# Kernel optimization log

Measured on AMD Instinct MI355X. Metric: run time of the kernel, lower is better.

The kernel has to match this reference:

```python
import jax, jax.numpy as jnp
import numpy as np

B, N, D, H = 8, 1024, 1024, 16
HD = D // H  # head_size = 64


def setup_inputs() -> dict:
    key = jax.random.key(0)
    k0, k1, k2, k3, k4 = jax.random.split(key, 5)
    scale = 1.0 / np.sqrt(D)
    return {
        "x": jax.random.normal(k0, (B, N, D), dtype=jnp.float32),
        "Wqkv": jax.random.normal(k1, (D, 3 * D), dtype=jnp.float32) * scale,
        "bqkv": jnp.zeros((3 * D,), dtype=jnp.float32),
        "Wo": jax.random.normal(k2, (D, D), dtype=jnp.float32) * scale,
        "bo": jnp.zeros((D,), dtype=jnp.float32),
    }


def reference(x, Wqkv, bqkv, Wo, bo):
    # Fused QKV projection: [B, N, 3D]
    qkv = jnp.einsum("bnd,de->bne", x, Wqkv) + bqkv
    q, k, v = jnp.split(qkv, 3, axis=-1)

    def split_heads(t):  # [B, N, D] -> [B, H, N, HD]
        return t.reshape(B, N, H, HD).transpose(0, 2, 1, 3)

    q, k, v = split_heads(q), split_heads(k), split_heads(v)

    # Scaled dot-product attention (no mask, dropout=0)
    scores = jnp.einsum("bhqd,bhkd->bhqk", q, k) / jnp.sqrt(jnp.float32(HD))
    alpha = jax.nn.softmax(scores, axis=-1)
    ctx = jnp.einsum("bhqk,bhkd->bhqd", alpha, v)  # [B, H, N, HD]

    ctx = ctx.transpose(0, 2, 1, 3).reshape(B, N, D)
    out = jnp.einsum("bnd,de->bne", ctx, Wo) + bo
    return out
```

## Files before the change

kernel.cpp:

```cpp
#include <hip/hip_runtime.h>
#include <cstdint>
#include <cstddef>

typedef _Float16 half_t;
typedef __attribute__((ext_vector_type(4))) _Float16 half4v;
typedef __attribute__((ext_vector_type(8))) _Float16 half8v;
typedef __attribute__((ext_vector_type(4))) float float4v;
typedef __attribute__((ext_vector_type(16))) float float16v;
typedef __attribute__((ext_vector_type(4))) unsigned uint4v;
typedef __attribute__((ext_vector_type(2))) int int2v;

typedef __attribute__((address_space(1))) const void gv_t;
typedef __attribute__((address_space(3))) void lv_t;

__device__ __forceinline__ void lds_cp16(const void* g, void* l) {
  __builtin_amdgcn_global_load_lds((gv_t*)g, (lv_t*)l, 16, 0, 0);
}

__device__ __forceinline__ unsigned pkh(float a, float b) {
  return __builtin_bit_cast(unsigned, __builtin_amdgcn_cvt_pkrtz(a, b));
}

__global__ __launch_bounds__(256) void k_cvt(const float* __restrict__ in,
                                             half_t* __restrict__ out) {
  int i = blockIdx.x * 256 + threadIdx.x;
  float4 v = ((const float4*)in)[i];
  half4v h = {(half_t)v.x, (half_t)v.y, (half_t)v.z, (half_t)v.w};
  ((half4v*)out)[i] = h;
}

__global__ __launch_bounds__(256) void k_tcvt(const float* __restrict__ in,
                                              half_t* __restrict__ out, int R, int C) {
  __shared__ float t[32][33];
  int c0 = blockIdx.x * 32, r0 = blockIdx.y * 32;
  int tc = threadIdx.x & 31, tr = threadIdx.x >> 5;
#pragma unroll
  for (int i = 0; i < 4; i++)
    t[tr + i * 8][tc] = in[(size_t)(r0 + tr + i * 8) * C + c0 + tc];
  __syncthreads();
#pragma unroll
  for (int i = 0; i < 4; i++)
    out[(size_t)(c0 + tr + i * 8) * R + r0 + tc] = (half_t)t[tc][tr + i * 8];
}

__global__ __launch_bounds__(256, 3) void k_qkv(
    const half_t* __restrict__ A, const half_t* __restrict__ Bt,
    const float* __restrict__ bias,
    half_t* __restrict__ Qo, half_t* __restrict__ Ko, half_t* __restrict__ Vo) {
  __shared__ half_t Bs[2][128 * 64];
  const int tid = threadIdx.x;
  const int lane = tid & 63;
  const int w = tid >> 6;
  const int xcd = blockIdx.x & 7;
  const int l = blockIdx.x >> 3;
  const int nc = l >> 6, r = l & 63;
  const int m0 = (xcd * 8 + (r >> 3)) * 128;
  const int n0 = (nc * 8 + (r & 7)) * 128;
  const int wr = w >> 1, wc = w & 1;
  const int fr = lane & 15, fg = lane >> 4;

  int sr[4], sg[4];
#pragma unroll
  for (int j = 0; j < 4; ++j) {
    const int G = j * 256 + tid;
    sr[j] = G >> 3;
    sg[j] = (G & 7) ^ (sr[j] & 7);
  }

  const half_t* Ap = A + (size_t)(m0 + wr * 64 + fr) * 1024 + fg * 8;

  float4v acc[4][4] = {};
  const int so0 = fg ^ (fr & 7);
  const int so1 = (4 | fg) ^ (fr & 7);
  const int brow = wc * 64 + fr;

  half8v a0[8], a1[8];
#pragma unroll
  for (int j = 0; j < 4; ++j)
    lds_cp16(Bt + (size_t)(n0 + sr[j]) * 1024 + sg[j] * 8, &Bs[0][(j * 256 + tid) * 8]);
#pragma unroll
  for (int m = 0; m < 4; ++m)
#pragma unroll
    for (int kk = 0; kk < 2; ++kk)
      a0[m * 2 + kk] = *(const half8v*)(Ap + m * 16384 + kk * 32);
  asm volatile("s_waitcnt vmcnt(0)" ::: "memory");
  __builtin_amdgcn_s_barrier();

#define QKV_ITER(t, cb, ac, an)                                                  \
  do {                                                                           \
    if ((t) + 1 < 16) {                                                          \
      const int kn = ((t) + 1) * 64;                                             \
      _Pragma("unroll") for (int j = 0; j < 4; ++j)                              \
          lds_cp16(Bt + (size_t)(n0 + sr[j]) * 1024 + kn + sg[j] * 8,            \
                   &Bs[(cb) ^ 1][(j * 256 + tid) * 8]);                          \
      _Pragma("unroll") for (int m = 0; m < 4; ++m)                              \
          _Pragma("unroll") for (int kk = 0; kk < 2; ++kk)                       \
              an[m * 2 + kk] = *(const half8v*)(Ap + m * 16384 + kn + kk * 32);  \
    }                                                                            \
    _Pragma("unroll") for (int kk = 0; kk < 2; ++kk) {                           \
      half8v b[4];                                                               \
      _Pragma("unroll") for (int n = 0; n < 4; ++n) {                            \
        const int row = (brow + n * 16) * 64;                                    \
        b[n] = *(const half8v*)(&Bs[cb][row + (kk ? so1 : so0) * 8]);            \
      }                                                                          \
      _Pragma("unroll") for (int m = 0; m < 4; ++m)                              \
          _Pragma("unroll") for (int n = 0; n < 4; ++n)                          \
              acc[m][n] = __builtin_amdgcn_mfma_f32_16x16x32_f16(                \
                  ac[m * 2 + kk], b[n], acc[m][n], 0, 0, 0);                     \
    }                                                                            \
    asm volatile("s_waitcnt vmcnt(0)" ::: "memory");                             \
    __builtin_amdgcn_s_barrier();                                                \
  } while (0)

  for (int tp = 0; tp < 8; ++tp) {
    QKV_ITER(2 * tp, 0, a0, a1);
    QKV_ITER(2 * tp + 1, 1, a1, a0);
  }
#undef QKV_ITER

  const int rq = (lane >> 4) * 4;
  const int cc = lane & 15;
#pragma unroll
  for (int n = 0; n < 4; n++) {
    const int e = n0 + wc * 64 + n * 16 + cc;
    const float bv = bias[e];
    const int which = e >> 10, h = (e >> 6) & 15, hd = e & 63;
#pragma unroll
    for (int m = 0; m < 4; m++) {
      const int rowb = m0 + wr * 64 + m * 16 + rq;
#pragma unroll
      for (int r2 = 0; r2 < 4; r2++) {
        const int row = rowb + r2;
        const int b_ = row >> 10, tok = row & 1023;
        const half_t hv = (half_t)(acc[m][n][r2] + bv);
        const size_t bh = (size_t)(b_ * 16 + h);
        if (which == 0)
          Qo[(bh * 1024 + tok) * 64 + hd] = hv;
        else if (which == 1)
          Ko[(bh * 1024 + tok) * 64 + hd] = hv;
        else
          Vo[(bh * 64 + hd) * 1024 + tok] = hv;
      }
    }
  }
}

__global__ __launch_bounds__(256, 2) void k_gemm_o(
    const half_t* __restrict__ A, const half_t* __restrict__ Bt,
    const float* __restrict__ bias, float* __restrict__ Cout, int N, int K) {
  __shared__ half_t As[2][128 * 64];
  __shared__ half_t Bs[2][128 * 64];
  const int tid = threadIdx.x;
  const int lane = tid & 63;
  const int w = tid >> 6;
  const int xcd = blockIdx.x & 7;
  const int l = blockIdx.x >> 3;
  const int nc = l >> 6, r = l & 63;
  const int m0 = (xcd * 8 + (r >> 3)) * 128;
  const int n0 = (nc * 8 + (r & 7)) * 128;
  const int wr = w >> 1, wc = w & 1;

  int sr[4], sg[4];
#pragma unroll
  for (int j = 0; j < 4; ++j) {
    const int G = j * 256 + tid;
    sr[j] = G >> 3;
    sg[j] = (G & 7) ^ (sr[j] & 7);
  }

  float4v acc[4][4] = {};
  const int fr = lane & 15;
  const int fg = lane >> 4;
  const int so0 = fg ^ (fr & 7);
  const int so1 = (4 | fg) ^ (fr & 7);
  const int arow = wr * 64 + fr;
  const int brow = wc * 64 + fr;

  const int NT = K >> 6;
#pragma unroll
  for (int j = 0; j < 4; ++j) {
    lds_cp16(A + (size_t)(m0 + sr[j]) * K + sg[j] * 8, &As[0][(j * 256 + tid) * 8]);
    lds_cp16(Bt + (size_t)(n0 + sr[j]) * K + sg[j] * 8, &Bs[0][(j * 256 + tid) * 8]);
  }

  for (int t = 0; t < NT; t++) {
    asm volatile("s_waitcnt vmcnt(0)" ::: "memory");
    __builtin_amdgcn_s_barrier();
    __builtin_amdgcn_sched_barrier(0);
    const int cb = t & 1;
    if (t + 1 < NT) {
      const int kn = (t + 1) * 64;
#pragma unroll
      for (int j = 0; j < 4; ++j) {
        lds_cp16(A + (size_t)(m0 + sr[j]) * K + kn + sg[j] * 8,
                 &As[cb ^ 1][(j * 256 + tid) * 8]);
        lds_cp16(Bt + (size_t)(n0 + sr[j]) * K + kn + sg[j] * 8,
                 &Bs[cb ^ 1][(j * 256 + tid) * 8]);
      }
    }
    half8v a[4][2], b[4][2];
#pragma unroll
    for (int m = 0; m < 4; m++) {
      const int row = (arow + m * 16) * 64;
      a[m][0] = *(const half8v*)(&As[cb][row + so0 * 8]);
      a[m][1] = *(const half8v*)(&As[cb][row + so1 * 8]);
    }
#pragma unroll
    for (int n = 0; n < 4; n++) {
      const int row = (brow + n * 16) * 64;
      b[n][0] = *(const half8v*)(&Bs[cb][row + so0 * 8]);
      b[n][1] = *(const half8v*)(&Bs[cb][row + so1 * 8]);
    }
#pragma unroll
    for (int kk = 0; kk < 2; kk++)
#pragma unroll
      for (int m = 0; m < 4; m++)
#pragma unroll
        for (int n = 0; n < 4; n++)
          acc[m][n] = __builtin_amdgcn_mfma_f32_16x16x32_f16(a[m][kk], b[n][kk],
                                                             acc[m][n], 0, 0, 0);
  }

  const int rq = (lane >> 4) * 4;
  const int cc = lane & 15;
#pragma unroll
  for (int n = 0; n < 4; n++) {
    int e = n0 + wc * 64 + n * 16 + cc;
    float bv = bias[e];
#pragma unroll
    for (int m = 0; m < 4; m++) {
      int rowb = m0 + wr * 64 + m * 16 + rq;
#pragma unroll
      for (int r2 = 0; r2 < 4; r2++)
        Cout[(size_t)(rowb + r2) * N + e] = acc[m][n][r2] + bv;
    }
  }
}

__global__ __launch_bounds__(512, 4) void k_attn(const half_t* __restrict__ Qh,
                                                 const half_t* __restrict__ Kh,
                                                 const half_t* __restrict__ Vt,
                                                 half_t* __restrict__ ctx) {
  __shared__ alignas(16) half_t Ks[2][64 * 64];
  __shared__ alignas(16) half_t Vs[2][64 * 64];
  const int lane = threadIdx.x & 63;
  const int w = threadIdx.x >> 6;
  const int ql = lane & 31, hi = lane >> 5;
  const int xcd = blockIdx.x & 7, loc = blockIdx.x >> 3;
  const int bh = xcd * 16 + (loc >> 2), qb = loc & 3;
  const int b_ = bh >> 4, h = bh & 15;
  const int q0 = qb * 256 + w * 32;

  const half_t* Qp = Qh + (size_t)bh * (1024 * 64);
  const half_t* Kp = Kh + (size_t)bh * (1024 * 64);
  const half_t* Vp = Vt + (size_t)bh * (64 * 1024);

  half8v qf[4];
#pragma unroll
  for (int c = 0; c < 4; c++) {
    half8v tq = *(const half8v*)(Qp + (size_t)(q0 + ql) * 64 + c * 16 + hi * 8);
    qf[c] = tq * (_Float16)0.125f;
  }

  const int G = w * 64 + lane;
  const int rS = G >> 3;
  const int gS = (G & 7) ^ (rS & 7);

  float16v co[2] = {};
  float mr = -1e30f, ssum = 0.f;

  lds_cp16(Kp + (size_t)rS * 64 + gS * 8, &Ks[0][w * 512]);
  lds_cp16(Vp + (size_t)rS * 1024 + 0 + gS * 8, &Vs[0][w * 512]);
  __syncthreads();

  int cur = 0;
  for (int t = 0; t < 16; t++) {
    if (t < 15) {
      const int kn = (t + 1) * 64;
      lds_cp16(Kp + (size_t)(kn + rS) * 64 + gS * 8, &Ks[cur ^ 1][w * 512]);
      lds_cp16(Vp + (size_t)rS * 1024 + kn + gS * 8, &Vs[cur ^ 1][w * 512]);
    }

    float16v sacc[2] = {};
    __builtin_amdgcn_s_setprio(1);
#pragma unroll
    for (int c = 0; c < 4; c++)
#pragma unroll
      for (int s = 0; s < 2; s++) {
        int row = s * 32 + ql;
        half8v kf = *(const half8v*)(&Ks[cur][row * 64 + (((2 * c + hi) ^ (row & 7)) * 8)]);
        sacc[s] = __builtin_amdgcn_mfma_f32_32x32x16_f16(kf, qf[c], sacc[s], 0, 0, 0);
      }
    __builtin_amdgcn_s_setprio(0);

    float mx = -1e30f;
#pragma unroll
    for (int s = 0; s < 2; s++)
#pragma unroll
      for (int i = 0; i < 16; i++) mx = fmaxf(mx, sacc[s][i]);
    mx = fmaxf(mx, __shfl_xor(mx, 32, 64));
    if (mx > mr + 8.f) {
      float fac = __expf(mr - mx);
      mr = mx;
      ssum *= fac;
#pragma unroll
      for (int dd = 0; dd < 2; dd++)
#pragma unroll
        for (int i = 0; i < 16; i++) co[dd][i] *= fac;
    }
    float rsum = 0.f;
#pragma unroll
    for (int s = 0; s < 2; s++)
#pragma unroll
      for (int i = 0; i < 16; i++) {
        float e = __expf(sacc[s][i] - mr);
        sacc[s][i] = e;
        rsum += e;
      }
    rsum += __shfl_xor(rsum, 32, 64);
    ssum += rsum;

#pragma unroll
    for (int kc = 0; kc < 4; kc++) {
      const int s = kc >> 1, o = (kc & 1) * 8;
      unsigned dA0 = pkh(sacc[s][o + 0], sacc[s][o + 1]);
      unsigned dA1 = pkh(sacc[s][o + 2], sacc[s][o + 3]);
      unsigned dB0 = pkh(sacc[s][o + 4], sacc[s][o + 5]);
      unsigned dB1 = pkh(sacc[s][o + 6], sacc[s][o + 7]);
      int2v r0 = __builtin_amdgcn_permlane32_swap((int)dA0, (int)dB0, false, false);
      int2v r1 = __builtin_amdgcn_permlane32_swap((int)dA1, (int)dB1, false, false);
      uint4v pw = {(unsigned)r0.x, (unsigned)r1.x, (unsigned)r0.y, (unsigned)r1.y};
      half8v pf = __builtin_bit_cast(half8v, pw);
      __builtin_amdgcn_s_setprio(1);
#pragma unroll
      for (int dd = 0; dd < 2; dd++) {
        int row = dd * 32 + ql;
        half8v vf = *(const half8v*)(&Vs[cur][row * 64 + (((2 * kc + hi) ^ (row & 7)) * 8)]);
        co[dd] = __builtin_amdgcn_mfma_f32_32x32x16_f16(vf, pf, co[dd], 0, 0, 0);
      }
      __builtin_amdgcn_s_setprio(0);
    }
    __syncthreads();
    cur ^= 1;
  }

  float rinv = 1.0f / ssum;
  half_t* outp = ctx + ((size_t)(b_ * 1024 + q0 + ql) * 1024 + h * 64);
#pragma unroll
  for (int dd = 0; dd < 2; dd++)
#pragma unroll
    for (int g = 0; g < 4; g++) {
      int d0 = dd * 32 + g * 8 + hi * 4;
      unsigned p0 = pkh(co[dd][g * 4 + 0] * rinv, co[dd][g * 4 + 1] * rinv);
      unsigned p1 = pkh(co[dd][g * 4 + 2] * rinv, co[dd][g * 4 + 3] * rinv);
      *(unsigned*)(outp + d0) = p0;
      *(unsigned*)(outp + d0 + 2) = p1;
    }
}

extern "C" void kernel_launch(void* const* d_in, const int* in_sizes, int n_in,
                              void* d_out, int out_size, void* d_ws, size_t ws_size,
                              hipStream_t stream) {
  const float* x = (const float*)d_in[0];
  const float* Wqkv = (const float*)d_in[1];
  const float* bqkv = (const float*)d_in[2];
  const float* Wo = (const float*)d_in[3];
  const float* bo = (const float*)d_in[4];
  float* out = (float*)d_out;
  char* ws = (char*)d_ws;

  const size_t NEED = 75497472;
  if (ws_size < NEED) return;
  half_t* xh = (half_t*)(ws);
  half_t* wqkvT = (half_t*)(ws + 16777216);
  half_t* woT = (half_t*)(ws + 23068672);
  half_t* Qh = (half_t*)(ws + 25165824);
  half_t* Kh = (half_t*)(ws + 41943040);
  half_t* Vt = (half_t*)(ws + 58720256);
  half_t* ctxh = xh;

  k_cvt<<<8192, 256, 0, stream>>>(x, xh);
  k_tcvt<<<dim3(96, 32), 256, 0, stream>>>(Wqkv, wqkvT, 1024, 3072);
  k_tcvt<<<dim3(32, 32), 256, 0, stream>>>(Wo, woT, 1024, 1024);
  k_qkv<<<1536, 256, 0, stream>>>(xh, wqkvT, bqkv, Qh, Kh, Vt);
  k_attn<<<512, 512, 0, stream>>>(Qh, Kh, Vt, ctxh);
  k_gemm_o<<<512, 256, 0, stream>>>(ctxh, woT, bo, out, 1024, 1024);
}
```

Baseline: 211.9 us.

## Make QKV GEMM persistent over three N tiles with LDS-staged A

The QKV projection kernel now launches 512 blocks instead of 1536, and each block loops over three 128-wide output column tiles for the same 128-row A tile. A is staged through double-buffered LDS with global_load_lds instead of going straight to registers, and results are written out after every 16 K-steps. MFMA sections in both GEMMs are wrapped with s_setprio to favour the compute phase. The aim is better L2 reuse of A and fewer waves in flight, at the cost of lower occupancy (launch bounds drop to 2 blocks per CU) and a longer serial loop per block.

After: 172.0 us. 1.23x faster.

```diff
diff --git a/kernel.cpp b/kernel.cpp
--- a/kernel.cpp
+++ b/kernel.cpp
@@ -43,19 +43,19 @@
     out[(size_t)(c0 + tr + i * 8) * R + r0 + tc] = (half_t)t[tc][tr + i * 8];
 }
 
-__global__ __launch_bounds__(256, 3) void k_qkv(
+__global__ __launch_bounds__(256, 2) void k_qkv(
     const half_t* __restrict__ A, const half_t* __restrict__ Bt,
     const float* __restrict__ bias,
     half_t* __restrict__ Qo, half_t* __restrict__ Ko, half_t* __restrict__ Vo) {
+  __shared__ half_t As[2][128 * 64];
   __shared__ half_t Bs[2][128 * 64];
   const int tid = threadIdx.x;
   const int lane = tid & 63;
   const int w = tid >> 6;
   const int xcd = blockIdx.x & 7;
-  const int l = blockIdx.x >> 3;
-  const int nc = l >> 6, r = l & 63;
-  const int m0 = (xcd * 8 + (r >> 3)) * 128;
-  const int n0 = (nc * 8 + (r & 7)) * 128;
+  const int loc = blockIdx.x >> 3;
+  const int m0 = (xcd * 8 + (loc & 7)) * 128;
+  const int nbase = loc >> 3;
   const int wr = w >> 1, wc = w & 1;
   const int fr = lane & 15, fg = lane >> 4;
 
@@ -67,80 +67,92 @@
     sg[j] = (G & 7) ^ (sr[j] & 7);
   }
 
-  const half_t* Ap = A + (size_t)(m0 + wr * 64 + fr) * 1024 + fg * 8;
-
   float4v acc[4][4] = {};
+
   const int so0 = fg ^ (fr & 7);
   const int so1 = (4 | fg) ^ (fr & 7);
+  const int arow = wr * 64 + fr;
   const int brow = wc * 64 + fr;
-
-  half8v a0[8], a1[8];
-#pragma unroll
-  for (int j = 0; j < 4; ++j)
-    lds_cp16(Bt + (size_t)(n0 + sr[j]) * 1024 + sg[j] * 8, &Bs[0][(j * 256 + tid) * 8]);
-#pragma unroll
-  for (int m = 0; m < 4; ++m)
-#pragma unroll
-    for (int kk = 0; kk < 2; ++kk)
-      a0[m * 2 + kk] = *(const half8v*)(Ap + m * 16384 + kk * 32);
-  asm volatile("s_waitcnt vmcnt(0)" ::: "memory");
-  __builtin_amdgcn_s_barrier();
-
-#define QKV_ITER(t, cb, ac, an)                                                  \
-  do {                                                                           \
-    if ((t) + 1 < 16) {                                                          \
-      const int kn = ((t) + 1) * 64;                                             \
-      _Pragma("unroll") for (int j = 0; j < 4; ++j)                              \
-          lds_cp16(Bt + (size_t)(n0 + sr[j]) * 1024 + kn + sg[j] * 8,            \
-                   &Bs[(cb) ^ 1][(j * 256 + tid) * 8]);                          \
-      _Pragma("unroll") for (int m = 0; m < 4; ++m)                              \
-          _Pragma("unroll") for (int kk = 0; kk < 2; ++kk)                       \
-              an[m * 2 + kk] = *(const half8v*)(Ap + m * 16384 + kn + kk * 32);  \
-    }                                                                            \
-    _Pragma("unroll") for (int kk = 0; kk < 2; ++kk) {                           \
-      half8v b[4];                                                               \
-      _Pragma("unroll") for (int n = 0; n < 4; ++n) {                            \
-        const int row = (brow + n * 16) * 64;                                    \
-        b[n] = *(const half8v*)(&Bs[cb][row + (kk ? so1 : so0) * 8]);            \
-      }                                                                          \
-      _Pragma("unroll") for (int m = 0; m < 4; ++m)                              \
-          _Pragma("unroll") for (int n = 0; n < 4; ++n)                          \
-              acc[m][n] = __builtin_amdgcn_mfma_f32_16x16x32_f16(                \
-                  ac[m * 2 + kk], b[n], acc[m][n], 0, 0, 0);                     \
-    }                                                                            \
-    asm volatile("s_waitcnt vmcnt(0)" ::: "memory");                             \
-    __builtin_amdgcn_s_barrier();                                                \
-  } while (0)
-
-  for (int tp = 0; tp < 8; ++tp) {
-    QKV_ITER(2 * tp, 0, a0, a1);
-    QKV_ITER(2 * tp + 1, 1, a1, a0);
-  }
-#undef QKV_ITER
-
   const int rq = (lane >> 4) * 4;
   const int cc = lane & 15;
-#pragma unroll
-  for (int n = 0; n < 4; n++) {
-    const int e = n0 + wc * 64 + n * 16 + cc;
-    const float bv = bias[e];
-    const int which = e >> 10, h = (e >> 6) & 15, hd = e & 63;
+
+#pragma unroll
+  for (int j = 0; j < 4; ++j) {
+    lds_cp16(A + (size_t)(m0 + sr[j]) * 1024 + sg[j] * 8, &As[0][(j * 256 + tid) * 8]);
+    lds_cp16(Bt + (size_t)(nbase * 128 + sr[j]) * 1024 + sg[j] * 8,
+             &Bs[0][(j * 256 + tid) * 8]);
+  }
+
+  for (int T = 0; T < 48; ++T) {
+    asm volatile("s_waitcnt vmcnt(0)" ::: "memory");
+    __builtin_amdgcn_s_barrier();
+    __builtin_amdgcn_sched_barrier(0);
+    const int cb = T & 1;
+    if (T + 1 < 48) {
+      const int Tn = T + 1;
+      const int kn = (Tn & 15) * 64;
+      const int n0n = (nbase + (Tn >> 4) * 8) * 128;
+#pragma unroll
+      for (int j = 0; j < 4; ++j) {
+        lds_cp16(A + (size_t)(m0 + sr[j]) * 1024 + kn + sg[j] * 8,
+                 &As[cb ^ 1][(j * 256 + tid) * 8]);
+        lds_cp16(Bt + (size_t)(n0n + sr[j]) * 1024 + kn + sg[j] * 8,
+                 &Bs[cb ^ 1][(j * 256 + tid) * 8]);
+      }
+    }
+    half8v a[4][2], b[4][2];
 #pragma unroll
     for (int m = 0; m < 4; m++) {
-      const int rowb = m0 + wr * 64 + m * 16 + rq;
-#pragma unroll
-      for (int r2 = 0; r2 < 4; r2++) {
-        const int row = rowb + r2;
-        const int b_ = row >> 10, tok = row & 1023;
-        const half_t hv = (half_t)(acc[m][n][r2] + bv);
-        const size_t bh = (size_t)(b_ * 16 + h);
-        if (which == 0)
-          Qo[(bh * 1024 + tok) * 64 + hd] = hv;
-        else if (which == 1)
-          Ko[(bh * 1024 + tok) * 64 + hd] = hv;
-        else
-          Vo[(bh * 64 + hd) * 1024 + tok] = hv;
-      }
+      const int row = (arow + m * 16) * 64;
+      a[m][0] = *(const half8v*)(&As[cb][row + so0 * 8]);
+      a[m][1] = *(const half8v*)(&As[cb][row + so1 * 8]);
+    }
+#pragma unroll
+    for (int n = 0; n < 4; n++) {
+      const int row = (brow + n * 16) * 64;
+      b[n][0] = *(const half8v*)(&Bs[cb][row + so0 * 8]);
+      b[n][1] = *(const half8v*)(&Bs[cb][row + so1 * 8]);
+    }
+    __builtin_amdgcn_s_setprio(1);
+#pragma unroll
+    for (int kk = 0; kk < 2; kk++)
+#pragma unroll
+      for (int m = 0; m < 4; m++)
+#pragma unroll
+        for (int n = 0; n < 4; n++)
+          acc[m][n] = __builtin_amdgcn_mfma_f32_16x16x32_f16(a[m][kk], b[n][kk],
+                                                             acc[m][n], 0, 0, 0);
+    __builtin_amdgcn_s_setprio(0);
+
+    if ((T & 15) == 15) {
+      const int n0 = (nbase + (T >> 4) * 8) * 128;
+#pragma unroll
+      for (int n = 0; n < 4; n++) {
+        const int e = n0 + wc * 64 + n * 16 + cc;
+        const float bv = bias[e];
+        const int which = e >> 10, h = (e >> 6) & 15, hd = e & 63;
+#pragma unroll
+        for (int m = 0; m < 4; m++) {
+          const int rowb = m0 + wr * 64 + m * 16 + rq;
+#pragma unroll
+          for (int r2 = 0; r2 < 4; r2++) {
+            const int row = rowb + r2;
+            const int b_ = row >> 10, tok = row & 1023;
+            const half_t hv = (half_t)(acc[m][n][r2] + bv);
+            const size_t bh = (size_t)(b_ * 16 + h);
+            if (which == 0)
+              Qo[(bh * 1024 + tok) * 64 + hd] = hv;
+            else if (which == 1)
+              Ko[(bh * 1024 + tok) * 64 + hd] = hv;
+            else
+              Vo[(bh * 64 + hd) * 1024 + tok] = hv;
+          }
+        }
+      }
+#pragma unroll
+      for (int m = 0; m < 4; m++)
+#pragma unroll
+        for (int n = 0; n < 4; n++) acc[m][n] = (float4v){0.f, 0.f, 0.f, 0.f};
     }
   }
 }
@@ -211,6 +223,7 @@
       b[n][0] = *(const half8v*)(&Bs[cb][row + so0 * 8]);
       b[n][1] = *(const half8v*)(&Bs[cb][row + so1 * 8]);
     }
+    __builtin_amdgcn_s_setprio(1);
 #pragma unroll
     for (int kk = 0; kk < 2; kk++)
 #pragma unroll
@@ -219,6 +232,7 @@
         for (int n = 0; n < 4; n++)
           acc[m][n] = __builtin_amdgcn_mfma_f32_16x16x32_f16(a[m][kk], b[n][kk],
                                                              acc[m][n], 0, 0, 0);
+    __builtin_amdgcn_s_setprio(0);
   }
 
   const int rq = (lane >> 4) * 4;
@@ -382,7 +396,7 @@
   k_cvt<<<8192, 256, 0, stream>>>(x, xh);
   k_tcvt<<<dim3(96, 32), 256, 0, stream>>>(Wqkv, wqkvT, 1024, 3072);
   k_tcvt<<<dim3(32, 32), 256, 0, stream>>>(Wo, woT, 1024, 1024);
-  k_qkv<<<1536, 256, 0, stream>>>(xh, wqkvT, bqkv, Qh, Kh, Vt);
+  k_qkv<<<512, 256, 0, stream>>>(xh, wqkvT, bqkv, Qh, Kh, Vt);
   k_attn<<<512, 512, 0, stream>>>(Qh, Kh, Vt, ctxh);
   k_gemm_o<<<512, 256, 0, stream>>>(ctxh, woT, bo, out, 1024, 1024);
 }
```
